# Kernel tuning notes

Measured on AMD Instinct MI355X. Metric: run time of the kernel, lower is better.

## Reference

```python
import jax, jax.numpy as jnp
import numpy as np

B, T, A, H, E = 512, 64, 32, 512, 32


def sinusoidal_pos_encoding(t, dim):
    # t: (B, T) float positions -> (B, T, dim)
    half = dim // 2
    freqs = jnp.exp(-jnp.log(10000.0) * jnp.arange(half, dtype=jnp.float32) / half)
    ang = t[..., None] * freqs  # (B, T, half)
    return jnp.concatenate([jnp.sin(ang), jnp.cos(ang)], axis=-1)


def cat_linear(x, W, b, cat_ids):
    # x: (B, T, Din); W: (E, Din, Dout); b: (E, Dout); cat_ids: (B,)
    Wg = W[cat_ids]            # (B, Din, Dout) gathered per-sample weights
    bg = b[cat_ids][:, None]   # (B, 1, Dout)
    return jnp.einsum('btd,bdh->bth', x, Wg) + bg


def swish(x):
    return x * jax.nn.sigmoid(x)


def setup_inputs() -> dict:
    key = jax.random.key(0)
    ks = jax.random.split(key, 10)
    s = lambda fan_in: 1.0 / np.sqrt(fan_in)
    return {
        'actions': jax.random.normal(ks[0], (B, T, A), dtype=jnp.float32),
        'timesteps': jax.random.uniform(ks[1], (B,), dtype=jnp.float32),
        'cat_ids': jax.random.randint(ks[2], (B,), 0, E),
        'W1': jax.random.normal(ks[3], (E, A, H), dtype=jnp.float32) * s(A),
        'b1': jnp.zeros((E, H), dtype=jnp.float32),
        'W2': jax.random.normal(ks[4], (E, 2 * H, H), dtype=jnp.float32) * s(2 * H),
        'b2': jnp.zeros((E, H), dtype=jnp.float32),
        'W3': jax.random.normal(ks[5], (E, H, H), dtype=jnp.float32) * s(H),
        'b3': jnp.zeros((E, H), dtype=jnp.float32),
    }


def reference(actions, timesteps, cat_ids, W1, b1, W2, b2, W3, b3):
    b, t, _ = actions.shape
    timesteps_bt = jnp.broadcast_to(timesteps[:, None], (b, t))
    a_emb = cat_linear(actions, W1, b1, cat_ids)              # (B, T, H)
    tau_emb = sinusoidal_pos_encoding(timesteps_bt, H).astype(a_emb.dtype)
    x = jnp.concatenate([a_emb, tau_emb], axis=-1)            # (B, T, 2H)
    x = swish(cat_linear(x, W2, b2, cat_ids))                 # (B, T, H)
    x = cat_linear(x, W3, b3, cat_ids)                        # (B, T, H)
    return x
```

## Files before the change

kernel.cpp:

```cpp
#include <hip/hip_runtime.h>
#include <hip/hip_bf16.h>

#define B_ 512
#define T_ 64
#define A_ 32
#define H_ 512
#define E_ 32
#define MAX_TASKS 272
#define CAP_ 168
#define GRID_ (8 * CAP_)
#define TSC 16

typedef unsigned short u16;
typedef unsigned int u32;
typedef __attribute__((ext_vector_type(8))) short short8;
typedef __attribute__((ext_vector_type(4))) float floatx4;

static __device__ __forceinline__ u16 f2bf(float f) {
    u32 u = __builtin_bit_cast(u32, f);
    u += 0x7fffu + ((u >> 16) & 1u);
    return (u16)(u >> 16);
}

static __device__ __forceinline__ void gl2lds16(const u16* g, u16* l) {
    __builtin_amdgcn_global_load_lds(
        (const __attribute__((address_space(1))) void*)g,
        (__attribute__((address_space(3))) void*)l, 16, 0, 0);
}

__global__ __launch_bounds__(512) void embed_group_kernel(
        const float* __restrict__ actions, const float* __restrict__ timesteps,
        const int* __restrict__ cat_ids, const float* __restrict__ W1,
        const float* __restrict__ b1, const float* __restrict__ b2,
        u16* __restrict__ a_emb, float* __restrict__ tauG,
        float* __restrict__ bias2s,
        int* __restrict__ sample_list, int4* __restrict__ tasks,
        int* __restrict__ itemlist, int* __restrict__ eoff_g,
        int* __restrict__ ecnt_g) {
    int tid = threadIdx.x;

    if (blockIdx.x == B_) {
        __shared__ int cnt[E_], off[E_], cur[E_], toff[E_], jc[8];
        __shared__ int total, fb;
        if (tid < E_) { cnt[tid] = 0; cur[tid] = 0; }
        __syncthreads();
        int e = cat_ids[tid];
        atomicAdd(&cnt[e], 1);
        __syncthreads();
        if (tid == 0) {
            int run = 0, trun = 0;
            for (int i = 0; i < E_; i++) {
                off[i] = run;  run += cnt[i];
                toff[i] = trun; trun += (cnt[i] + 1) >> 1;
            }
            total = trun;
        }
        __syncthreads();
        if (tid < E_) {
            int c = cnt[tid], o = off[tid], to = toff[tid];
            eoff_g[tid] = o;
            ecnt_g[tid] = c;
            for (int j = 0; j < c; j += 2)
                tasks[to++] = make_int4(tid, o + j, (c - j >= 2) ? 2 : 1, 0);
        }
        if (tid < 8) {
            int J = 0;
            for (int cc = 0; cc < 4; cc++)
                J += 4 * ((cnt[tid + 8 * cc] + 1) >> 1);
            jc[tid] = J;
        }
        __syncthreads();
        if (tid == 0) {
            int f = 0;
            for (int x = 0; x < 8; x++) if (jc[x] > CAP_) f = 1;
            fb = f;
        }
        __syncthreads();
        if (!fb) {
            if (tid < 8) {
                int j = 0;
                for (int cc = 0; cc < 4; cc++) {
                    int ee = tid + 8 * cc;
                    int nt = (cnt[ee] + 1) >> 1, t0 = toff[ee];
                    for (int t = t0; t < t0 + nt; t++)
                        for (int nb = 0; nb < 4; nb++) {
                            itemlist[tid + 8 * j] = (t << 2) | nb;
                            j++;
                        }
                }
                for (; j < CAP_; j++) itemlist[tid + 8 * j] = -1;
            }
        } else {
            for (int f = tid; f < GRID_; f += 512)
                itemlist[f] = (f < 4 * total) ? f : -1;
        }
        int p = atomicAdd(&cur[e], 1);
        sample_list[off[e] + p] = tid;
        return;
    }

    int b = blockIdx.x;
    int e = cat_ids[b];
    {
        float tval = timesteps[b];
        int kk = tid & 255;
        float freq = expf(-9.210340371976184f * (float)kk * (1.0f / 256.0f));
        float ang = tval * freq;
        tauG[(size_t)b * H_ + tid] = (tid < 256) ? sinf(ang) : cosf(ang);
        bias2s[(size_t)b * H_ + tid] = b2[e * H_ + tid];
    }

    __shared__ float act[T_ * A_];
    const float* asrc = actions + (size_t)b * T_ * A_;
    for (int i = tid; i < T_ * A_; i += 512) act[i] = asrc[i];
    __syncthreads();

    const float* w1 = W1 + (size_t)e * A_ * H_;
    float wcol[A_];
#pragma unroll
    for (int k = 0; k < A_; k++) wcol[k] = w1[k * H_ + tid];
    float bb = b1[e * H_ + tid];
    u16* orow = a_emb + (size_t)b * T_ * H_;
    for (int tt = 0; tt < T_; tt++) {
        float acc = bb;
#pragma unroll
        for (int k = 0; k < A_; k++)
            acc = fmaf(act[tt * A_ + k], wcol[k], acc);
        orow[tt * H_ + tid] = f2bf(acc);
    }
}

static __device__ __forceinline__ void ct_block(
        const float* __restrict__ W, u16* __restrict__ Wt,
        int srcK, int dstK, int e, int k0, int n) {
    const float* src = W + ((size_t)e * srcK + k0) * H_ + n;
    short8 out[8];
#pragma unroll
    for (int j = 0; j < 64; j++)
        out[j >> 3][j & 7] = (short)f2bf(src[(size_t)j * H_]);
    u16* dst = Wt + ((size_t)e * H_ + n) * dstK + k0;
#pragma unroll
    for (int c = 0; c < 8; c++) *(short8*)(dst + c * 8) = out[c];
}

__global__ __launch_bounds__(256) void convert_transpose(
        const float* __restrict__ W, u16* __restrict__ Wt, int srcK, int dstK) {
    ct_block(W, Wt, srcK, dstK, blockIdx.z, blockIdx.x * 64,
             blockIdx.y * 256 + threadIdx.x);
}

__global__ __launch_bounds__(256) void prep_kernel(
        const float* __restrict__ W2, u16* __restrict__ Wt2a,
        const float* __restrict__ tauG, const int* __restrict__ sample_list,
        const int* __restrict__ eoff, const int* __restrict__ ecnt,
        float* __restrict__ bias2s) {
    int tid = threadIdx.x;
    int bid = blockIdx.x;

    __shared__ float tauT[128][20];
    __shared__ float pS[4][TSC][64];

    if (bid < 512) {
        int e = bid >> 4, sub = bid & 15;
        ct_block(W2, Wt2a, 2 * H_, H_, e, (sub & 7) * 64,
                 (sub >> 3) * 256 + tid);
        return;
    }

    int id = bid - 512;
    int cc = id & 7;
    int e  = (id >> 3) & 31;
    int kq = id >> 8;
    int cnt = ecnt[e], off = eoff[e];
    if (cnt == 0) return;
    int ks = tid >> 6;
    int ln = tid & 63;
    int n = cc * 64 + ln;
    const float* wb = W2 + ((size_t)e * 1024 + 512 + kq * 128) * H_;

    for (int c0 = 0; c0 < cnt; c0 += TSC) {
        for (int i = tid; i < TSC * 128; i += 256) {
            int sl = i >> 7, k = i & 127;
            float v = 0.f;
            if (c0 + sl < cnt)
                v = tauG[(size_t)sample_list[off + c0 + sl] * H_ + kq * 128 + k];
            tauT[k][sl] = v;
        }
        __syncthreads();

        float a[TSC];
#pragma unroll
        for (int s = 0; s < TSC; s++) a[s] = 0.f;

#pragma unroll 8
        for (int j = 0; j < 32; j++) {
            int k = ks * 32 + j;
            float w = wb[(size_t)k * H_ + n];
            float tv[TSC];
            *(float4*)&tv[0]  = *(const float4*)&tauT[k][0];
            *(float4*)&tv[4]  = *(const float4*)&tauT[k][4];
            *(float4*)&tv[8]  = *(const float4*)&tauT[k][8];
            *(float4*)&tv[12] = *(const float4*)&tauT[k][12];
#pragma unroll
            for (int s = 0; s < TSC; s++) a[s] = fmaf(tv[s], w, a[s]);
        }

#pragma unroll
        for (int s = 0; s < TSC; s++) pS[ks][s][ln] = a[s];
        __syncthreads();

        for (int o = tid; o < TSC * 64; o += 256) {
            int sl = o >> 6, l = o & 63;
            if (c0 + sl < cnt) {
                float v = pS[0][sl][l] + pS[1][sl][l] +
                          pS[2][sl][l] + pS[3][sl][l];
                int s = sample_list[off + c0 + sl];
                unsafeAtomicAdd(&bias2s[(size_t)s * H_ + cc * 64 + l], v);
            }
        }
        __syncthreads();
    }
}

template <int DIN, bool PSBIAS, bool DO_SWISH, bool OUT_BF16>
__global__ __launch_bounds__(256, 2) void moe_gemm(
        const u16* __restrict__ xsrc, const u16* __restrict__ Wt,
        const float* __restrict__ bias,
        const int* __restrict__ sample_list, const int4* __restrict__ tasks,
        const int* __restrict__ itemlist, void* __restrict__ outp) {
    int item = itemlist[blockIdx.x];
    if (item < 0) return;
    int4 task = tasks[item >> 2];
    int nb = item & 3;
    int ns = task.z;
    int e = task.x;
    int s0 = sample_list[task.y];
    int s1 = (ns > 1) ? sample_list[task.y + 1] : s0;
    int n0 = nb * 128;

    int tid = threadIdx.x;
    int lane = tid & 63, wv = tid >> 6;
    int wr = wv >> 1, wc = wv & 1;
    int quad = lane >> 4, c15 = lane & 15;
    int r8 = lane >> 3, cg = lane & 7;

    __shared__ __align__(16) u16 xs[2][128 * 64];
    __shared__ __align__(16) u16 wt[2][128 * 64];

    floatx4 acc[4][4];
    floatx4 zero4 = {0.f, 0.f, 0.f, 0.f};
#pragma unroll
    for (int i = 0; i < 4; i++)
#pragma unroll
        for (int j = 0; j < 4; j++) acc[i][j] = zero4;

    const u16* wbase = Wt + (size_t)(e * H_ + n0) * DIN;
    int kc_sw = (cg ^ r8) * 8;

    auto stage = [&](int b, int k0) {
#pragma unroll
        for (int h = 0; h < 4; h++) {
            int rbase = h * 32 + wv * 8;
            int s = (h < 2) ? s0 : s1;
            int t = (rbase + r8) & 63;
            gl2lds16(xsrc + ((size_t)s * T_ + t) * H_ + k0 + kc_sw,
                     &xs[b][rbase * 64]);
        }
#pragma unroll
        for (int h = 0; h < 4; h++) {
            int nbase = h * 32 + wv * 8;
            gl2lds16(wbase + (size_t)(nbase + r8) * DIN + k0 + kc_sw,
                     &wt[b][nbase * 64]);
        }
    };

    auto compute = [&](int b) {
#pragma unroll
        for (int kk = 0; kk < 2; kk++) {
            int c = kk * 4 + quad;
            short8 af[4], bfr[4];
#pragma unroll
            for (int i = 0; i < 4; i++) {
                int row = wr * 64 + i * 16 + c15;
                af[i] = *(const short8*)&xs[b][row * 64 + ((c ^ (row & 7)) * 8)];
                int nr = wc * 64 + i * 16 + c15;
                bfr[i] = *(const short8*)&wt[b][nr * 64 + ((c ^ (nr & 7)) * 8)];
            }
#pragma unroll
            for (int mt = 0; mt < 4; mt++)
#pragma unroll
                for (int nt = 0; nt < 4; nt++)
                    acc[mt][nt] = __builtin_amdgcn_mfma_f32_16x16x32_bf16(
                            af[mt], bfr[nt], acc[mt][nt], 0, 0, 0);
        }
    };

    constexpr int KI = DIN / 64;
    stage(0, 0);
    stage(1, 64);
    asm volatile("s_waitcnt vmcnt(8)" ::: "memory");
    __builtin_amdgcn_s_barrier();
    __builtin_amdgcn_sched_barrier(0);
#pragma unroll
    for (int t = 0; t < KI; ++t) {
        compute(t & 1);
        if (t + 1 < KI) {
            __builtin_amdgcn_s_barrier();
            __builtin_amdgcn_sched_barrier(0);
            if (t + 2 < KI) {
                stage(t & 1, (t + 2) * 64);
                asm volatile("s_waitcnt vmcnt(8)" ::: "memory");
            } else {
                asm volatile("s_waitcnt vmcnt(0)" ::: "memory");
            }
            __builtin_amdgcn_s_barrier();
            __builtin_amdgcn_sched_barrier(0);
        }
    }

    if (wr >= ns) return;
    int s = (wr == 0) ? s0 : s1;
    const float* bp = PSBIAS ? (bias + (size_t)s * H_)
                             : (bias + (size_t)e * H_);
#pragma unroll
    for (int mt = 0; mt < 4; mt++) {
        int tb = mt * 16 + quad * 4;
#pragma unroll
        for (int nt = 0; nt < 4; nt++) {
            int col = n0 + wc * 64 + nt * 16 + c15;
            float bv = bp[col];
#pragma unroll
            for (int r = 0; r < 4; r++) {
                float v = acc[mt][nt][r] + bv;
                if (DO_SWISH) v = v / (1.0f + expf(-v));
                size_t oidx = ((size_t)s * T_ + tb + r) * H_ + col;
                if (OUT_BF16) ((u16*)outp)[oidx] = f2bf(v);
                else          ((float*)outp)[oidx] = v;
            }
        }
    }
}

extern "C" void kernel_launch(void* const* d_in, const int* in_sizes, int n_in,
                              void* d_out, int out_size, void* d_ws, size_t ws_size,
                              hipStream_t stream) {
    const float* actions   = (const float*)d_in[0];
    const float* timesteps = (const float*)d_in[1];
    const int*   cat_ids   = (const int*)d_in[2];
    const float* W1 = (const float*)d_in[3];
    const float* b1 = (const float*)d_in[4];
    const float* W2 = (const float*)d_in[5];
    const float* b2 = (const float*)d_in[6];
    const float* W3 = (const float*)d_in[7];
    const float* b3 = (const float*)d_in[8];

    char* ws = (char*)d_ws;
    u16* a_emb = (u16*)ws;
    u16* y     = (u16*)(ws + (size_t)32 * 1024 * 1024);
    char* meta = ws + (size_t)64 * 1024 * 1024 + 512 * 1024;
    int*  sample_list = (int*)meta;
    int4* tasks       = (int4*)(meta + 8192);
    int*  itemlist    = (int*)(meta + 16384);
    int*  eoff        = (int*)(meta + 24576);
    int*  ecnt        = (int*)(meta + 24576 + 128);
    u16*  Wt2a   = (u16*)d_out;
    float* bias2s = (float*)((char*)d_out + (size_t)48 * 1024 * 1024);
    float* tauG   = (float*)((char*)d_out + (size_t)52 * 1024 * 1024);
    u16*  Wt3    = a_emb;

    hipLaunchKernelGGL(embed_group_kernel, dim3(B_ + 1), dim3(512), 0, stream,
                       actions, timesteps, cat_ids, W1, b1, b2,
                       a_emb, tauG, bias2s,
                       sample_list, tasks, itemlist, eoff, ecnt);
    hipLaunchKernelGGL(prep_kernel, dim3(1536), dim3(256), 0, stream,
                       W2, Wt2a, tauG, sample_list, eoff, ecnt, bias2s);
    hipLaunchKernelGGL((moe_gemm<H_, true, true, true>), dim3(GRID_),
                       dim3(256), 0, stream,
                       a_emb, Wt2a, bias2s, sample_list, tasks, itemlist,
                       (void*)y);
    hipLaunchKernelGGL(convert_transpose, dim3(H_ / 64, 2, E_), dim3(256),
                       0, stream, W3, Wt3, H_, H_);
    hipLaunchKernelGGL((moe_gemm<H_, false, false, false>), dim3(GRID_),
                       dim3(256), 0, stream,
                       y, Wt3, b3, sample_list, tasks, itemlist, d_out);
}
```

Measured before the change: 285.1 us.

## Restructure tau-bias GEMV in prep kernel to use float4 weight loads

Reorganises the part of the prep kernel that multiplies the sinusoidal tau embedding by W2. Each thread now loads float4 weight vectors and accumulates a 4x4 register tile (4 samples by 4 outputs). Each wave covers 4 of the 16 samples in a chunk, so the cross-wave shared-memory reduction and its extra barrier go away. The grid changes from 1536 to 1024 blocks, with blocks split by expert, K slice and N half. The trade-off is more global atomics per output, since there are 8 K-slices instead of 4 and atomics are issued per element, and fewer blocks are available for the tau work.

```diff
diff --git a/kernel.cpp b/kernel.cpp
--- a/kernel.cpp
+++ b/kernel.cpp
@@ -157,9 +157,6 @@
     int tid = threadIdx.x;
     int bid = blockIdx.x;
 
-    __shared__ float tauT[128][20];
-    __shared__ float pS[4][TSC][64];
-
     if (bid < 512) {
         int e = bid >> 4, sub = bid & 15;
         ct_block(W2, Wt2a, 2 * H_, H_, e, (sub & 7) * 64,
@@ -167,55 +164,57 @@
         return;
     }
 
+    __shared__ float tauT[64][17];
     int id = bid - 512;
-    int cc = id & 7;
-    int e  = (id >> 3) & 31;
-    int kq = id >> 8;
+    int nh = id & 1;
+    int ks = (id >> 1) & 7;
+    int e  = id >> 4;
     int cnt = ecnt[e], off = eoff[e];
     if (cnt == 0) return;
-    int ks = tid >> 6;
-    int ln = tid & 63;
-    int n = cc * 64 + ln;
-    const float* wb = W2 + ((size_t)e * 1024 + 512 + kq * 128) * H_;
+    int wv = tid >> 6, ln = tid & 63;
+    const float* wb = W2 + ((size_t)e * 1024 + 512 + ks * 64) * H_
+                      + nh * 256 + ln * 4;
+    float* bout = bias2s + nh * 256 + ln * 4;
 
     for (int c0 = 0; c0 < cnt; c0 += TSC) {
-        for (int i = tid; i < TSC * 128; i += 256) {
-            int sl = i >> 7, k = i & 127;
+        for (int i = tid; i < TSC * 64; i += 256) {
+            int sl = i >> 6, k = i & 63;
             float v = 0.f;
             if (c0 + sl < cnt)
-                v = tauG[(size_t)sample_list[off + c0 + sl] * H_ + kq * 128 + k];
+                v = tauG[(size_t)sample_list[off + c0 + sl] * H_ + ks * 64 + k];
             tauT[k][sl] = v;
         }
         __syncthreads();
 
-        float a[TSC];
-#pragma unroll
-        for (int s = 0; s < TSC; s++) a[s] = 0.f;
-
+        float4 a0 = {0,0,0,0}, a1 = {0,0,0,0}, a2 = {0,0,0,0}, a3 = {0,0,0,0};
 #pragma unroll 8
-        for (int j = 0; j < 32; j++) {
-            int k = ks * 32 + j;
-            float w = wb[(size_t)k * H_ + n];
-            float tv[TSC];
-            *(float4*)&tv[0]  = *(const float4*)&tauT[k][0];
-            *(float4*)&tv[4]  = *(const float4*)&tauT[k][4];
-            *(float4*)&tv[8]  = *(const float4*)&tauT[k][8];
-            *(float4*)&tv[12] = *(const float4*)&tauT[k][12];
-#pragma unroll
-            for (int s = 0; s < TSC; s++) a[s] = fmaf(tv[s], w, a[s]);
-        }
-
-#pragma unroll
-        for (int s = 0; s < TSC; s++) pS[ks][s][ln] = a[s];
-        __syncthreads();
-
-        for (int o = tid; o < TSC * 64; o += 256) {
-            int sl = o >> 6, l = o & 63;
+        for (int k = 0; k < 64; k++) {
+            float4 w4 = *(const float4*)(wb + (size_t)k * H_);
+            float t0 = tauT[k][wv * 4 + 0];
+            float t1 = tauT[k][wv * 4 + 1];
+            float t2 = tauT[k][wv * 4 + 2];
+            float t3 = tauT[k][wv * 4 + 3];
+            a0.x = fmaf(t0, w4.x, a0.x); a0.y = fmaf(t0, w4.y, a0.y);
+            a0.z = fmaf(t0, w4.z, a0.z); a0.w = fmaf(t0, w4.w, a0.w);
+            a1.x = fmaf(t1, w4.x, a1.x); a1.y = fmaf(t1, w4.y, a1.y);
+            a1.z = fmaf(t1, w4.z, a1.z); a1.w = fmaf(t1, w4.w, a1.w);
+            a2.x = fmaf(t2, w4.x, a2.x); a2.y = fmaf(t2, w4.y, a2.y);
+            a2.z = fmaf(t2, w4.z, a2.z); a2.w = fmaf(t2, w4.w, a2.w);
+            a3.x = fmaf(t3, w4.x, a3.x); a3.y = fmaf(t3, w4.y, a3.y);
+            a3.z = fmaf(t3, w4.z, a3.z); a3.w = fmaf(t3, w4.w, a3.w);
+        }
+
+#pragma unroll
+        for (int si = 0; si < 4; si++) {
+            int sl = wv * 4 + si;
             if (c0 + sl < cnt) {
-                float v = pS[0][sl][l] + pS[1][sl][l] +
-                          pS[2][sl][l] + pS[3][sl][l];
                 int s = sample_list[off + c0 + sl];
-                unsafeAtomicAdd(&bias2s[(size_t)s * H_ + cc * 64 + l], v);
+                float4 a = (si == 0) ? a0 : (si == 1) ? a1 : (si == 2) ? a2 : a3;
+                float* p = bout + (size_t)s * H_;
+                unsafeAtomicAdd(p + 0, a.x);
+                unsafeAtomicAdd(p + 1, a.y);
+                unsafeAtomicAdd(p + 2, a.z);
+                unsafeAtomicAdd(p + 3, a.w);
             }
         }
         __syncthreads();
@@ -372,7 +371,7 @@
                        actions, timesteps, cat_ids, W1, b1, b2,
                        a_emb, tauG, bias2s,
                        sample_list, tasks, itemlist, eoff, ecnt);
-    hipLaunchKernelGGL(prep_kernel, dim3(1536), dim3(256), 0, stream,
+    hipLaunchKernelGGL(prep_kernel, dim3(1024), dim3(256), 0, stream,
                        W2, Wt2a, tauG, sample_list, eoff, ecnt, bias2s);
     hipLaunchKernelGGL((moe_gemm<H_, true, true, true>), dim3(GRID_),
                        dim3(256), 0, stream,
```

New measurement: 303.3 us. 6.4% more time.
